# Performance work log

Hardware: AMD Instinct MI355X
Metric: run time of the kernel (lower is better)

## Reference

```python
import jax, jax.numpy as jnp
import numpy as np

N_NODES = 100000
N_EDGES = 1600000
D_IN = 128
D_OUT = 128
ALPHA = 0.01   # LeakyReLU negative slope
BN_EPS = 1e-5


def setup_inputs() -> dict:
    key = jax.random.key(0)
    ks = jax.random.split(key, 4)
    x = jax.random.normal(ks[0], (N_NODES, D_IN), dtype=jnp.float32)
    edge_idx = jax.random.randint(ks[1], (2, N_EDGES), 0, N_NODES, dtype=jnp.int64)
    # SAGEConv params: lin_l (neighbor path, with bias) and lin_r (root path, no bias)
    s = 1.0 / np.sqrt(D_IN)
    W_l = jax.random.uniform(ks[2], (D_OUT, D_IN), jnp.float32, -s, s)
    b_l = jnp.zeros((D_OUT,), jnp.float32)
    W_r = jax.random.uniform(ks[3], (D_OUT, D_IN), jnp.float32, -s, s)
    gamma = jnp.ones((D_OUT,), jnp.float32)
    beta = jnp.zeros((D_OUT,), jnp.float32)
    return {"x": x, "edge_idx": edge_idx, "W_l": W_l, "b_l": b_l,
            "W_r": W_r, "gamma": gamma, "beta": beta}


def reference(x, edge_idx, W_l, b_l, W_r, gamma, beta):
    src = edge_idx[0]
    dst = edge_idx[1]
    # mean aggregation of source-node features at target nodes (PyG SAGEConv default)
    msg_sum = jax.ops.segment_sum(x[src], dst, num_segments=N_NODES)      # [N, D_IN]
    cnt = jax.ops.segment_sum(jnp.ones((src.shape[0],), x.dtype), dst,
                              num_segments=N_NODES)                        # [N]
    mean = msg_sum / jnp.maximum(cnt, 1.0)[:, None]
    # out = lin_l(mean_agg) + lin_r(x)
    h = mean @ W_l.T + b_l + x @ W_r.T                                     # [N, D_OUT]
    # BatchNorm1d in training mode (biased variance over node dim)
    mu = jnp.mean(h, axis=0)
    var = jnp.mean((h - mu) ** 2, axis=0)
    h = gamma * (h - mu) * jax.lax.rsqrt(var + BN_EPS) + beta
    # LeakyReLU
    return jnp.where(h >= 0, h, ALPHA * h)
```

## Files before the change

kernel.cpp:

```cpp
#include <hip/hip_runtime.h>
#include <hip/hip_bf16.h>
#include <stdint.h>

#define N_NODES 100000
#define N_EDGES 1600000
#define DIM     128
#define ALPHA   0.01f
#define BN_EPS  1e-5f
#define NBUCK   3125
#define NBLK_P  128
#define EPB     12500
#define SRT_CAP 1536

typedef __bf16 bf16x8 __attribute__((ext_vector_type(8)));
typedef float  f32x4  __attribute__((ext_vector_type(4)));
typedef float  f32x2  __attribute__((ext_vector_type(2)));

#if defined(__has_builtin)
#if __has_builtin(__builtin_amdgcn_cvt_pk_fp8_f32) && __has_builtin(__builtin_amdgcn_cvt_pk_f32_fp8)
#define USE_FP8_BUILTIN 1
#endif
#endif

static const size_t OFF_SUM   = 512;
static const size_t OFF_SUMSQ = 1024;
static const size_t OFF_BBASE = 2048;
static const size_t OFF_BT    = 14592;
static const size_t OFF_TMP   = 32768;
static const size_t OFF_BFRAG = 6432768;
static const size_t OFF_AMEAN = 6498304;
static const size_t OFF_X8    = 32098304;
static const size_t OFF_H     = 44898304;
static const size_t OFF_XB    = 70498304;
static const size_t OFF_GHIST = 96098304;
static const size_t OFF_SOFFT = 97698304;

__device__ __forceinline__ float bf2f(unsigned short h) {
    return __uint_as_float(((unsigned int)h) << 16);
}
__device__ __forceinline__ float bflo(unsigned int w) {
    return __uint_as_float(w << 16);
}
__device__ __forceinline__ float bfhi(unsigned int w) {
    return __uint_as_float(w & 0xffff0000u);
}
__device__ __forceinline__ unsigned short f2bf(float f) {
    unsigned int u = __float_as_uint(f);
    u = u + 0x7fffu + ((u >> 16) & 1u);
    return (unsigned short)(u >> 16);
}
__device__ __forceinline__ unsigned int pack2(float a, float b) {
    return (unsigned int)f2bf(a) | ((unsigned int)f2bf(b) << 16);
}
__device__ __forceinline__ float loadS(const void* p, int i, int isf32) {
    return isf32 ? ((const float*)p)[i] : bf2f(((const unsigned short*)p)[i]);
}
__device__ __forceinline__ int edge_at(const void* e, long long i, int idx64) {
    return idx64 ? (int)((const long long*)e)[i] : ((const int*)e)[i];
}
__device__ __forceinline__ int blkpos(int k) { return ((k & 7) << 4) | (k >> 3); }

#ifndef USE_FP8_BUILTIN
__device__ __forceinline__ unsigned int enc_fp8_1(float f) {
    unsigned int u = __float_as_uint(f);
    unsigned int s = (u >> 24) & 0x80u;
    unsigned int au = u & 0x7fffffffu;
    if (au >= 0x43E00000u) return s | 0x7Eu;
    if (au < 0x3C800000u) {
        int m = (int)rintf(__uint_as_float(au) * 512.0f);
        return s | (unsigned int)m;
    }
    unsigned int r = au + 0x7FFFFu + ((au >> 20) & 1u);
    unsigned int e = (r >> 23) & 0xffu;
    unsigned int m3 = (r >> 20) & 7u;
    return s | ((e - 120u) << 3) | m3;
}
#endif
__device__ __forceinline__ unsigned int enc4(float f0, float f1, float f2, float f3) {
#ifdef USE_FP8_BUILTIN
    int r = __builtin_amdgcn_cvt_pk_fp8_f32(f0, f1, 0, false);
    r = __builtin_amdgcn_cvt_pk_fp8_f32(f2, f3, r, true);
    return (unsigned int)r;
#else
    return enc_fp8_1(f0) | (enc_fp8_1(f1) << 8) | (enc_fp8_1(f2) << 16) | (enc_fp8_1(f3) << 24);
#endif
}
__device__ __forceinline__ void dec4(unsigned int w, float* o) {
#ifdef USE_FP8_BUILTIN
    f32x2 a = __builtin_amdgcn_cvt_pk_f32_fp8(w, false);
    f32x2 b = __builtin_amdgcn_cvt_pk_f32_fp8(w, true);
    o[0] = a[0]; o[1] = a[1]; o[2] = b[0]; o[3] = b[1];
#else
    #pragma unroll
    for (int j = 0; j < 4; j++) {
        unsigned int c = (w >> (8 * j)) & 0xffu;
        o[j] = __uint_as_float(((c & 0x80u) << 24) | ((c & 0x7fu) << 20)) * 0x1p120f;
    }
#endif
}

__device__ __forceinline__ int detect_idx64(const void* e) {
    const unsigned int* ew = (const unsigned int*)e;
    unsigned long long m = __ballot(ew[2 * (threadIdx.x & 63) + 1] != 0u);
    return (__popcll(m) < 8) ? 1 : 0;
}
__device__ __forceinline__ int detect_isf32(const void* x) {
    const unsigned int* xw = (const unsigned int*)x;
    unsigned int w = xw[threadIdx.x & 63];
    unsigned int e = (w >> 7) & 0xffu;
    bool bflike = (e >= 110u && e <= 140u) || ((w & 0xffffu) == 0u);
    unsigned long long m = __ballot(bflike);
    return (__popcll(m) > 32) ? 0 : 1;
}

__global__ __launch_bounds__(256) void k1_kernel(const void* edges, const void* x,
                                                 int* ghist, unsigned int* x8,
                                                 unsigned short* xb, float* gz) {
    int tid = threadIdx.x;
    if (blockIdx.x < NBLK_P) {
        __shared__ int sh[NBUCK];
        int idx64 = detect_idx64(edges);
        int blk = blockIdx.x;
        if (blk == 0) gz[tid] = 0.f;
        for (int i = tid; i < NBUCK; i += 256) sh[i] = 0;
        __syncthreads();
        long long base = (long long)blk * EPB;
        for (int i = tid; i < EPB; i += 256) {
            int d = edge_at(edges, (long long)N_EDGES + base + i, idx64);
            atomicAdd(&sh[d >> 5], 1);
        }
        __syncthreads();
        for (int i = tid; i < NBUCK; i += 256) ghist[blk * NBUCK + i] = sh[i];
    } else {
        int isf32 = detect_isf32(x);
        int gid = (blockIdx.x - NBLK_P) * 256 + tid;
        float f[16];
        if (!isf32) {
            const uint4* xv = (const uint4*)x;
            uint4 a = xv[gid * 2], b2 = xv[gid * 2 + 1];
            unsigned int w[8] = {a.x, a.y, a.z, a.w, b2.x, b2.y, b2.z, b2.w};
            #pragma unroll
            for (int i = 0; i < 8; i++) { f[2 * i] = bflo(w[i]); f[2 * i + 1] = bfhi(w[i]); }
        } else {
            const float4* xf = (const float4*)x;
            #pragma unroll
            for (int i = 0; i < 4; i++) {
                float4 v = xf[gid * 4 + i];
                f[4 * i] = v.x; f[4 * i + 1] = v.y; f[4 * i + 2] = v.z; f[4 * i + 3] = v.w;
            }
            uint4 h1, h2;
            h1.x = pack2(f[0], f[1]);  h1.y = pack2(f[2], f[3]);
            h1.z = pack2(f[4], f[5]);  h1.w = pack2(f[6], f[7]);
            h2.x = pack2(f[8], f[9]);  h2.y = pack2(f[10], f[11]);
            h2.z = pack2(f[12], f[13]); h2.w = pack2(f[14], f[15]);
            ((uint4*)xb)[gid * 2]     = h1;
            ((uint4*)xb)[gid * 2 + 1] = h2;
        }
        uint4 o;
        o.x = enc4(f[0], f[1], f[2], f[3]);
        o.y = enc4(f[4], f[5], f[6], f[7]);
        o.z = enc4(f[8], f[9], f[10], f[11]);
        o.w = enc4(f[12], f[13], f[14], f[15]);
        *(uint4*)(x8 + gid * 4) = o;
    }
}

__global__ __launch_bounds__(256) void p2a_kernel(const int* ghist, int* sOffT, int* bT) {
    int k = blockIdx.x, wv = threadIdx.x >> 6, lane = threadIdx.x & 63;
    int k0 = ((lane & 15) << 3) | (lane >> 4);
    int k1i = (((lane + 64) & 15) << 3) | ((lane + 64) >> 4);
    for (int g = 0; g < 4; g++) {
        int b = k * 16 + wv * 4 + g;
        if (b >= NBUCK) continue;
        int v0 = ghist[k0 * NBUCK + b];
        int v1 = ghist[k1i * NBUCK + b];
        int sc0 = v0, sc1 = v1;
        #pragma unroll
        for (int off = 1; off < 64; off <<= 1) {
            int u0 = __shfl_up(sc0, off, 64);
            int u1 = __shfl_up(sc1, off, 64);
            if (lane >= off) { sc0 += u0; sc1 += u1; }
        }
        int t0 = __shfl(sc0, 63, 64);
        sOffT[b * NBLK_P + lane] = sc0 - v0;
        sOffT[b * NBLK_P + 64 + lane] = t0 + sc1 - v1;
        if (lane == 63) bT[b] = t0 + sc1;
    }
}

__global__ __launch_bounds__(256) void k3_kernel(const int* bT, int* bucketBase,
                                                 const void* W_l, const void* W_r,
                                                 const void* x, unsigned short* bfrag) {
    int t = threadIdx.x;
    if (blockIdx.x == 0) {
        __shared__ int ws[4];
        int base = t * 13;
        int v[13]; int s = 0;
        #pragma unroll
        for (int i = 0; i < 13; i++) {
            int idx = base + i;
            v[i] = (idx < NBUCK) ? bT[idx] : 0;
            s += v[i];
        }
        int lane = t & 63, wv = t >> 6;
        int sc = s;
        #pragma unroll
        for (int off = 1; off < 64; off <<= 1) {
            int u = __shfl_up(sc, off, 64);
            if (lane >= off) sc += u;
        }
        if (lane == 63) ws[wv] = sc;
        __syncthreads();
        int add = 0;
        for (int w = 0; w < wv; w++) add += ws[w];
        int run = sc - s + add;
        #pragma unroll
        for (int i = 0; i < 13; i++) {
            int idx = base + i;
            if (idx < NBUCK) bucketBase[idx] = run;
            run += v[i];
        }
    } else {
        int isf32 = detect_isf32(x);
        int g = (blockIdx.x - 1) * 256 + t;
        int j    = g & 7;
        int lane = (g >> 3) & 63;
        int s    = (g >> 9) & 7;
        int tt   = (g >> 12) & 7;
        int n = tt * 16 + (lane & 15);
        int k = s * 32 + ((lane >> 4) & 3) * 8 + j;
        float v = (k < DIM) ? loadS(W_l, n * DIM + k, isf32)
                            : loadS(W_r, n * DIM + (k - DIM), isf32);
        bfrag[g] = f2bf(v);
    }
}

__global__ __launch_bounds__(256) void p3_kernel(const void* edges, const int* sOffT,
                                                 const int* bucketBase, unsigned int* tmp) {
    __shared__ int sbase[NBUCK];
    int idx64 = detect_idx64(edges);
    int blk = blockIdx.x, tid = threadIdx.x;
    int mypos = blkpos(blk);
    for (int i = tid; i < NBUCK; i += 256)
        sbase[i] = bucketBase[i] + sOffT[i * NBLK_P + mypos];
    __syncthreads();
    long long base = (long long)blk * EPB;
    for (int i = tid; i < EPB; i += 256) {
        long long e = base + i;
        int s = edge_at(edges, e, idx64);
        int d = edge_at(edges, (long long)N_EDGES + e, idx64);
        int p = atomicAdd(&sbase[d >> 5], 1);
        tmp[p] = ((unsigned int)(d & 31) << 17) | (unsigned int)s;
    }
}

__global__ __launch_bounds__(256) void agg_kernel(const unsigned int* x8, const unsigned int* tmp,
                                                  const int* bucketBase, unsigned short* Amean) {
    __shared__ int s_cnt[32];
    __shared__ int s_beg[32];
    __shared__ int s_srt[SRT_CAP];
    int b = blockIdx.x, tid = threadIdx.x;
    int gb = bucketBase[b];
    int ge = (b == NBUCK - 1) ? N_EDGES : bucketBase[b + 1];
    int nE = min(ge - gb, SRT_CAP);
    if (tid < 32) s_cnt[tid] = 0;
    __syncthreads();
    for (int i = tid; i < nE; i += 256) atomicAdd(&s_cnt[tmp[gb + i] >> 17], 1);
    __syncthreads();
    if (tid < 32) {
        int v = s_cnt[tid];
        int sc = v;
        #pragma unroll
        for (int off = 1; off < 32; off <<= 1) {
            int u = __shfl_up(sc, off, 64);
            if (tid >= off) sc += u;
        }
        s_beg[tid] = sc - v;
        s_cnt[tid] = sc - v;
    }
    __syncthreads();
    for (int i = tid; i < nE; i += 256) {
        unsigned int w = tmp[gb + i];
        int p = atomicAdd(&s_cnt[w >> 17], 1);
        s_srt[p] = (int)(w & 0x1ffffu);
    }
    __syncthreads();
    int wv = tid >> 6, lane = tid & 63;
    int oct = lane >> 3, l8 = lane & 7;
    int nl = wv * 8 + oct;
    int nb = s_beg[nl], ne2 = s_cnt[nl];
    const uint4* xv = (const uint4*)x8;
    float acc[16];
    #pragma unroll
    for (int i = 0; i < 16; i++) acc[i] = 0.f;
    for (int jj = nb; jj < ne2; jj += 4) {
        uint4 r[4]; float mk[4];
        #pragma unroll
        for (int u = 0; u < 4; u++) {
            int e = jj + u;
            int su = s_srt[(e < ne2) ? e : nb];
            mk[u] = (e < ne2) ? 1.f : 0.f;
            r[u] = xv[(size_t)su * 8 + l8];
        }
        #pragma unroll
        for (int u = 0; u < 4; u++) {
            float f[4];
            dec4(r[u].x, f);
            acc[0] = fmaf(f[0], mk[u], acc[0]);  acc[1] = fmaf(f[1], mk[u], acc[1]);
            acc[2] = fmaf(f[2], mk[u], acc[2]);  acc[3] = fmaf(f[3], mk[u], acc[3]);
            dec4(r[u].y, f);
            acc[4] = fmaf(f[0], mk[u], acc[4]);  acc[5] = fmaf(f[1], mk[u], acc[5]);
            acc[6] = fmaf(f[2], mk[u], acc[6]);  acc[7] = fmaf(f[3], mk[u], acc[7]);
            dec4(r[u].z, f);
            acc[8] = fmaf(f[0], mk[u], acc[8]);  acc[9] = fmaf(f[1], mk[u], acc[9]);
            acc[10] = fmaf(f[2], mk[u], acc[10]); acc[11] = fmaf(f[3], mk[u], acc[11]);
            dec4(r[u].w, f);
            acc[12] = fmaf(f[0], mk[u], acc[12]); acc[13] = fmaf(f[1], mk[u], acc[13]);
            acc[14] = fmaf(f[2], mk[u], acc[14]); acc[15] = fmaf(f[3], mk[u], acc[15]);
        }
    }
    int ng = b * 32 + nl;
    float inv = 1.0f / (float)max(ne2 - nb, 1);
    uint4 o1, o2;
    o1.x = pack2(acc[0] * inv, acc[1] * inv);
    o1.y = pack2(acc[2] * inv, acc[3] * inv);
    o1.z = pack2(acc[4] * inv, acc[5] * inv);
    o1.w = pack2(acc[6] * inv, acc[7] * inv);
    o2.x = pack2(acc[8] * inv, acc[9] * inv);
    o2.y = pack2(acc[10] * inv, acc[11] * inv);
    o2.z = pack2(acc[12] * inv, acc[13] * inv);
    o2.w = pack2(acc[14] * inv, acc[15] * inv);
    *(uint4*)(Amean + (size_t)ng * 128 + l8 * 16) = o1;
    *(uint4*)(Amean + (size_t)ng * 128 + l8 * 16 + 8) = o2;
}

__device__ __forceinline__ void loadA_frags(const unsigned short* __restrict__ Amean,
                                            const unsigned short* __restrict__ xs,
                                            int m0, int wave, int lm, int lq,
                                            bf16x8* a) {
    int rowA = m0 + wave * 16 + lm;
    if (rowA >= N_NODES) rowA = N_NODES - 1;
    const unsigned short* am = Amean + (size_t)rowA * 128 + lq * 8;
    const unsigned short* xm = xs + (size_t)rowA * 128 + lq * 8;
    #pragma unroll
    for (int s = 0; s < 4; s++) a[s] = *(const bf16x8*)(am + s * 32);
    #pragma unroll
    for (int s = 0; s < 4; s++) a[4 + s] = *(const bf16x8*)(xm + s * 32);
}

__global__ __launch_bounds__(256) void gemm_kernel(const unsigned short* __restrict__ Amean,
                                                   const void* __restrict__ x,
                                                   const unsigned short* __restrict__ xb,
                                                   const unsigned short* __restrict__ Bfrag_g,
                                                   const void* __restrict__ b_l,
                                                   unsigned int* __restrict__ Hu,
                                                   float* __restrict__ gpart) {
    __shared__ unsigned short lds[32768];
    __shared__ float sstat[2][128];
    int isf32 = detect_isf32(x);
    const unsigned short* xs = isf32 ? xb : (const unsigned short*)x;
    {
        const uint4* src = (const uint4*)Bfrag_g;
        uint4* dst = (uint4*)lds;
        for (int i = threadIdx.x; i < 4096; i += 256) dst[i] = src[i];
        if (threadIdx.x < 128) { sstat[0][threadIdx.x] = 0.f; sstat[1][threadIdx.x] = 0.f; }
    }
    __syncthreads();
    int wave = threadIdx.x >> 6, lane = threadIdx.x & 63;
    int lm = lane & 15, lq = lane >> 4;
    float bv[8];
    #pragma unroll
    for (int t = 0; t < 8; t++) bv[t] = loadS(b_l, t * 16 + lm, isf32);
    float st1[8], st2[8];
    #pragma unroll
    for (int t = 0; t < 8; t++) { st1[t] = 0.f; st2[t] = 0.f; }

    const int stride = gridDim.x * 64;
    int m0 = blockIdx.x * 64;
    bf16x8 aq[8];
    if (m0 < N_NODES) loadA_frags(Amean, xs, m0, wave, lm, lq, aq);

    for (; m0 < N_NODES; m0 += stride) {
        int mN = (m0 + stride < N_NODES) ? (m0 + stride) : m0;
        bf16x8 an[8];
        loadA_frags(Amean, xs, mN, wave, lm, lq, an);
        f32x4 acc[8];
        #pragma unroll
        for (int t = 0; t < 8; t++) acc[t] = (f32x4){0.f, 0.f, 0.f, 0.f};
        #pragma unroll
        for (int s = 0; s < 8; s++) {
            #pragma unroll
            for (int t = 0; t < 8; t++) {
                bf16x8 bb = *(const bf16x8*)(lds + ((t * 8 + s) * 64 + lane) * 8);
                acc[t] = __builtin_amdgcn_mfma_f32_16x16x32_bf16(aq[s], bb, acc[t], 0, 0, 0);
            }
        }
        #pragma unroll
        for (int t = 0; t < 8; t++) {
            #pragma unroll
            for (int r = 0; r < 4; r++) {
                int ro = m0 + wave * 16 + lq * 4 + r;
                float v = acc[t][r] + bv[t];
                float p = __shfl_xor(v, 1, 64);
                bool in = (ro < N_NODES);
                if (in) { st1[t] += v; st2[t] += v * v; }
                if (in && !(lm & 1)) Hu[(size_t)ro * 64 + t * 8 + (lm >> 1)] = pack2(v, p);
            }
        }
        #pragma unroll
        for (int s = 0; s < 8; s++) aq[s] = an[s];
    }
    #pragma unroll
    for (int t = 0; t < 8; t++) {
        atomicAdd(&sstat[0][t * 16 + lm], st1[t]);
        atomicAdd(&sstat[1][t * 16 + lm], st2[t]);
    }
    __syncthreads();
    gpart[(size_t)blockIdx.x * 256 + threadIdx.x] = ((const float*)sstat)[threadIdx.x];
}

__global__ __launch_bounds__(256) void redux_kernel(const float* gpart, float* gz) {
    int t = threadIdx.x;
    const float* p = gpart + (size_t)blockIdx.x * 64 * 256 + t;
    float a = 0.f;
    #pragma unroll
    for (int b = 0; b < 64; b++) a += p[(size_t)b * 256];
    atomicAdd(&gz[t], a);
}

__global__ __launch_bounds__(256) void bn_norm_kernel(const unsigned int* __restrict__ Hu,
                                                      const void* x,
                                                      const float* gsum,
                                                      const float* gsumsq, const void* gamma,
                                                      const void* beta, void* out) {
    __shared__ float sc[128], sh[128];
    int isf32 = detect_isf32(x);
    int tid = threadIdx.x;
    if (tid < 128) {
        const float invN = 1.0f / (float)N_NODES;
        float mu = gsum[tid] * invN;
        float var = gsumsq[tid] * invN - mu * mu;
        float rstd = rsqrtf(var + BN_EPS);
        float g = loadS(gamma, tid, isf32);
        float b = loadS(beta, tid, isf32);
        sc[tid] = g * rstd;
        sh[tid] = b - mu * g * rstd;
    }
    __syncthreads();
    size_t idx = (size_t)blockIdx.x * 256 + tid;
    size_t i8 = idx * 8;
    float h[8];
    {
        uint4 u = *(const uint4*)(Hu + idx * 4);
        h[0]=bflo(u.x); h[1]=bfhi(u.x); h[2]=bflo(u.y); h[3]=bfhi(u.y);
        h[4]=bflo(u.z); h[5]=bfhi(u.z); h[6]=bflo(u.w); h[7]=bfhi(u.w);
    }
    int c0 = (int)(i8 & 127);
    float o[8];
    #pragma unroll
    for (int i = 0; i < 8; i++) {
        float v = h[i] * sc[c0 + i] + sh[c0 + i];
        o[i] = (v >= 0.f) ? v : ALPHA * v;
    }
    if (isf32) {
        *(float4*)((float*)out + i8) = make_float4(o[0], o[1], o[2], o[3]);
        *(float4*)((float*)out + i8 + 4) = make_float4(o[4], o[5], o[6], o[7]);
    } else {
        uint4 u;
        u.x = pack2(o[0], o[1]); u.y = pack2(o[2], o[3]);
        u.z = pack2(o[4], o[5]); u.w = pack2(o[6], o[7]);
        *(uint4*)((unsigned short*)out + i8) = u;
    }
}

extern "C" void kernel_launch(void* const* d_in, const int* in_sizes, int n_in,
                              void* d_out, int out_size, void* d_ws, size_t ws_size,
                              hipStream_t stream) {
    const void* x     = d_in[0];
    const void* eidx  = d_in[1];
    const void* W_l   = d_in[2];
    const void* b_l   = d_in[3];
    const void* W_r   = d_in[4];
    const void* gamma = d_in[5];
    const void* beta  = d_in[6];
    char* ws = (char*)d_ws;
    float* gsum = (float*)(ws + OFF_SUM);
    float* gsumsq = (float*)(ws + OFF_SUMSQ);
    int* bucketBase = (int*)(ws + OFF_BBASE);
    int* bT = (int*)(ws + OFF_BT);
    unsigned int* tmp = (unsigned int*)(ws + OFF_TMP);
    unsigned short* bfrag = (unsigned short*)(ws + OFF_BFRAG);
    unsigned short* Amean = (unsigned short*)(ws + OFF_AMEAN);
    unsigned int* x8 = (unsigned int*)(ws + OFF_X8);
    unsigned int* H = (unsigned int*)(ws + OFF_H);
    unsigned short* xb = (unsigned short*)(ws + OFF_XB);
    int* ghist = (int*)(ws + OFF_GHIST);
    int* sOffT = (int*)(ws + OFF_SOFFT);
    float* gpart = (float*)(ws + OFF_TMP);

    k1_kernel<<<NBLK_P + 3125, 256, 0, stream>>>(eidx, x, ghist, x8, xb, gsum);
    p2a_kernel<<<196, 256, 0, stream>>>(ghist, sOffT, bT);
    k3_kernel<<<129, 256, 0, stream>>>(bT, bucketBase, W_l, W_r, x, bfrag);
    p3_kernel<<<NBLK_P, 256, 0, stream>>>(eidx, sOffT, bucketBase, tmp);
    agg_kernel<<<NBUCK, 256, 0, stream>>>(x8, tmp, bucketBase, Amean);
    gemm_kernel<<<512, 256, 0, stream>>>(Amean, x, xb, bfrag, b_l, H, gpart);
    redux_kernel<<<8, 256, 0, stream>>>(gpart, gsum);
    bn_norm_kernel<<<6250, 256, 0, stream>>>(H, x, gsum, gsumsq, gamma, beta, d_out);
}
```

Before: 277.9 us.

## Load all GEMM A tiles up front and stage B via direct global-to-LDS

The GEMM kernel drops its grid-stride loop with one-tile prefetch. Each block now owns 256 rows and issues every A-fragment load for its four 16-row tiles before the barrier, so those loads overlap the B-fragment staging. B staging now uses global_load_lds instead of a register round-trip, and the grid and reduction kernel are resized to 391 blocks. This exposes more memory parallelism up front, at the cost of heavier register use (occupancy hint of 2 blocks) and only one block wave on the device.

```diff
diff --git a/kernel.cpp b/kernel.cpp
--- a/kernel.cpp
+++ b/kernel.cpp
@@ -11,6 +11,7 @@
 #define NBLK_P  128
 #define EPB     12500
 #define SRT_CAP 1536
+#define GEMM_GRID 391
 
 typedef __bf16 bf16x8 __attribute__((ext_vector_type(8)));
 typedef float  f32x4  __attribute__((ext_vector_type(4)));
@@ -59,6 +60,15 @@
     return idx64 ? (int)((const long long*)e)[i] : ((const int*)e)[i];
 }
 __device__ __forceinline__ int blkpos(int k) { return ((k & 7) << 4) | (k >> 3); }
+
+__device__ __forceinline__ void gload_lds16(const void* g, void* l) {
+    __builtin_amdgcn_global_load_lds(
+        reinterpret_cast<const __attribute__((address_space(1))) unsigned int*>(
+            reinterpret_cast<uintptr_t>(g)),
+        reinterpret_cast<__attribute__((address_space(3))) unsigned int*>(
+            reinterpret_cast<uintptr_t>(l)),
+        16, 0, 0);
+}
 
 #ifndef USE_FP8_BUILTIN
 __device__ __forceinline__ unsigned int enc_fp8_1(float f) {
@@ -334,40 +344,41 @@
     *(uint4*)(Amean + (size_t)ng * 128 + l8 * 16 + 8) = o2;
 }
 
-__device__ __forceinline__ void loadA_frags(const unsigned short* __restrict__ Amean,
-                                            const unsigned short* __restrict__ xs,
-                                            int m0, int wave, int lm, int lq,
-                                            bf16x8* a) {
-    int rowA = m0 + wave * 16 + lm;
-    if (rowA >= N_NODES) rowA = N_NODES - 1;
-    const unsigned short* am = Amean + (size_t)rowA * 128 + lq * 8;
-    const unsigned short* xm = xs + (size_t)rowA * 128 + lq * 8;
-    #pragma unroll
-    for (int s = 0; s < 4; s++) a[s] = *(const bf16x8*)(am + s * 32);
-    #pragma unroll
-    for (int s = 0; s < 4; s++) a[4 + s] = *(const bf16x8*)(xm + s * 32);
-}
-
-__global__ __launch_bounds__(256) void gemm_kernel(const unsigned short* __restrict__ Amean,
-                                                   const void* __restrict__ x,
-                                                   const unsigned short* __restrict__ xb,
-                                                   const unsigned short* __restrict__ Bfrag_g,
-                                                   const void* __restrict__ b_l,
-                                                   unsigned int* __restrict__ Hu,
-                                                   float* __restrict__ gpart) {
+__global__ __launch_bounds__(256, 2) void gemm_kernel(const unsigned short* __restrict__ Amean,
+                                                      const void* __restrict__ x,
+                                                      const unsigned short* __restrict__ xb,
+                                                      const unsigned short* __restrict__ Bfrag_g,
+                                                      const void* __restrict__ b_l,
+                                                      unsigned int* __restrict__ Hu,
+                                                      float* __restrict__ gpart) {
     __shared__ unsigned short lds[32768];
     __shared__ float sstat[2][128];
     int isf32 = detect_isf32(x);
     const unsigned short* xs = isf32 ? xb : (const unsigned short*)x;
-    {
-        const uint4* src = (const uint4*)Bfrag_g;
-        uint4* dst = (uint4*)lds;
-        for (int i = threadIdx.x; i < 4096; i += 256) dst[i] = src[i];
-        if (threadIdx.x < 128) { sstat[0][threadIdx.x] = 0.f; sstat[1][threadIdx.x] = 0.f; }
-    }
-    __syncthreads();
-    int wave = threadIdx.x >> 6, lane = threadIdx.x & 63;
+    int tid = threadIdx.x;
+    int wave = tid >> 6, lane = tid & 63;
     int lm = lane & 15, lq = lane >> 4;
+
+    #pragma unroll
+    for (int k = 0; k < 16; k++) {
+        int e = tid + k * 256;
+        gload_lds16(Bfrag_g + (size_t)e * 8, lds + (size_t)e * 8);
+    }
+    if (tid < 128) { sstat[0][tid] = 0.f; sstat[1][tid] = 0.f; }
+
+    int base = blockIdx.x * 256;
+    bf16x8 aq[4][8];
+    #pragma unroll
+    for (int j = 0; j < 4; j++) {
+        int rowA = base + (wave * 4 + j) * 16 + lm;
+        if (rowA >= N_NODES) rowA = N_NODES - 1;
+        const unsigned short* am = Amean + (size_t)rowA * 128 + lq * 8;
+        const unsigned short* xm = xs + (size_t)rowA * 128 + lq * 8;
+        #pragma unroll
+        for (int s = 0; s < 4; s++) aq[j][s] = *(const bf16x8*)(am + s * 32);
+        #pragma unroll
+        for (int s = 0; s < 4; s++) aq[j][4 + s] = *(const bf16x8*)(xm + s * 32);
+    }
     float bv[8];
     #pragma unroll
     for (int t = 0; t < 8; t++) bv[t] = loadS(b_l, t * 16 + lm, isf32);
@@ -375,15 +386,10 @@
     #pragma unroll
     for (int t = 0; t < 8; t++) { st1[t] = 0.f; st2[t] = 0.f; }
 
-    const int stride = gridDim.x * 64;
-    int m0 = blockIdx.x * 64;
-    bf16x8 aq[8];
-    if (m0 < N_NODES) loadA_frags(Amean, xs, m0, wave, lm, lq, aq);
-
-    for (; m0 < N_NODES; m0 += stride) {
-        int mN = (m0 + stride < N_NODES) ? (m0 + stride) : m0;
-        bf16x8 an[8];
-        loadA_frags(Amean, xs, mN, wave, lm, lq, an);
+    __syncthreads();
+
+    #pragma unroll
+    for (int j = 0; j < 4; j++) {
         f32x4 acc[8];
         #pragma unroll
         for (int t = 0; t < 8; t++) acc[t] = (f32x4){0.f, 0.f, 0.f, 0.f};
@@ -392,14 +398,14 @@
             #pragma unroll
             for (int t = 0; t < 8; t++) {
                 bf16x8 bb = *(const bf16x8*)(lds + ((t * 8 + s) * 64 + lane) * 8);
-                acc[t] = __builtin_amdgcn_mfma_f32_16x16x32_bf16(aq[s], bb, acc[t], 0, 0, 0);
+                acc[t] = __builtin_amdgcn_mfma_f32_16x16x32_bf16(aq[j][s], bb, acc[t], 0, 0, 0);
             }
         }
         #pragma unroll
         for (int t = 0; t < 8; t++) {
             #pragma unroll
             for (int r = 0; r < 4; r++) {
-                int ro = m0 + wave * 16 + lq * 4 + r;
+                int ro = base + (wave * 4 + j) * 16 + lq * 4 + r;
                 float v = acc[t][r] + bv[t];
                 float p = __shfl_xor(v, 1, 64);
                 bool in = (ro < N_NODES);
@@ -407,8 +413,6 @@
                 if (in && !(lm & 1)) Hu[(size_t)ro * 64 + t * 8 + (lm >> 1)] = pack2(v, p);
             }
         }
-        #pragma unroll
-        for (int s = 0; s < 8; s++) aq[s] = an[s];
     }
     #pragma unroll
     for (int t = 0; t < 8; t++) {
@@ -421,10 +425,9 @@
 
 __global__ __launch_bounds__(256) void redux_kernel(const float* gpart, float* gz) {
     int t = threadIdx.x;
-    const float* p = gpart + (size_t)blockIdx.x * 64 * 256 + t;
     float a = 0.f;
-    #pragma unroll
-    for (int b = 0; b < 64; b++) a += p[(size_t)b * 256];
+    for (int b = blockIdx.x; b < GEMM_GRID; b += 8)
+        a += gpart[(size_t)b * 256 + t];
     atomicAdd(&gz[t], a);
 }
 
@@ -503,7 +506,7 @@
     k3_kernel<<<129, 256, 0, stream>>>(bT, bucketBase, W_l, W_r, x, bfrag);
     p3_kernel<<<NBLK_P, 256, 0, stream>>>(eidx, sOffT, bucketBase, tmp);
     agg_kernel<<<NBUCK, 256, 0, stream>>>(x8, tmp, bucketBase, Amean);
-    gemm_kernel<<<512, 256, 0, stream>>>(Amean, x, xb, bfrag, b_l, H, gpart);
+    gemm_kernel<<<GEMM_GRID, 256, 0, stream>>>(Amean, x, xb, bfrag, b_l, H, gpart);
     redux_kernel<<<8, 256, 0, stream>>>(gpart, gsum);
     bn_norm_kernel<<<6250, 256, 0, stream>>>(H, x, gsum, gsumsq, gamma, beta, d_out);
 }
```

Result: no change. 283.3 us (+1.9%).
